# Performance work log

Measured on AMD Instinct MI355X. Metric: run time of the kernel, lower is better.

Reference implementation:

```python
import jax, jax.numpy as jnp
import numpy as np
from jax import lax

DIM, HEADS, WS = 256, 8, 8
B, H, W = 2, 192, 192


def conv1x1(x, w, b):
    # x: (b,c,h,w), w: (o,c)
    return jnp.einsum('bchw,oc->bohw', x, w) + b[None, :, None, None]


def dwconv3x3(x, w, b):
    # w: (C,1,3,3), zeros padding (padding_mode='zeros')
    y = lax.conv_general_dilated(x, w, (1, 1), ((1, 1), (1, 1)),
                                 dimension_numbers=('NCHW', 'OIHW', 'NCHW'),
                                 feature_group_count=x.shape[1])
    return y + b[None, :, None, None]


def window_split(qkv):
    # (b, 3*heads*c, H, W) -> (3, b*h1*w1, heads, c, ws*ws)
    b, C3, h, w = qkv.shape
    c = C3 // (3 * HEADS)
    h1, w1 = h // WS, w // WS
    t = qkv.reshape(b, 3, HEADS, c, h1, WS, w1, WS)
    t = t.transpose(1, 0, 4, 6, 2, 3, 5, 7)  # (3,b,h1,w1,heads,c,ws,ws)
    return t.reshape(3, b * h1 * w1, HEADS, c, WS * WS)


def window_merge(o, b, h, w):
    # (b*h1*w1, heads, c, ws*ws) -> (b, heads*c, h, w)
    h1, w1 = h // WS, w // WS
    c = o.shape[2]
    t = o.reshape(b, h1, w1, HEADS, c, WS, WS)
    t = t.transpose(0, 3, 4, 1, 5, 2, 6)  # (b,heads,c,h1,ws,w1,ws)
    return t.reshape(b, HEADS * c, h, w)


def l2norm(x):
    n = jnp.linalg.norm(x, axis=-1, keepdims=True)
    return x / jnp.maximum(n, 1e-12)


def setup_inputs() -> dict:
    key = jax.random.key(0)
    ks = jax.random.split(key, 16)
    s = 0.02
    return {
        'x': jax.random.normal(ks[0], (B, DIM, H, W), jnp.float32),
        'x2': jax.random.normal(ks[1], (B, DIM, H, W), jnp.float32),
        'w_qkv': jax.random.normal(ks[2], (3 * DIM, DIM), jnp.float32) * s,
        'b_qkv': jnp.zeros((3 * DIM,), jnp.float32),
        'w_dw': jax.random.normal(ks[3], (3 * DIM, 1, 3, 3), jnp.float32) * s,
        'b_dw': jnp.zeros((3 * DIM,), jnp.float32),
        'w_qkv2': jax.random.normal(ks[4], (3 * DIM, DIM), jnp.float32) * s,
        'b_qkv2': jnp.zeros((3 * DIM,), jnp.float32),
        'w_dw2': jax.random.normal(ks[5], (3 * DIM, 1, 3, 3), jnp.float32) * s,
        'b_dw2': jnp.zeros((3 * DIM,), jnp.float32),
        'temp': jnp.ones((HEADS, 1, 1), jnp.float32) / np.sqrt(DIM).astype(np.float32),
        'w_proj': jax.random.normal(ks[6], (DIM, DIM), jnp.float32) * s,
        'b_proj': jnp.zeros((DIM,), jnp.float32),
    }


def reference(x, x2, w_qkv, b_qkv, w_dw, b_dw, w_qkv2, b_qkv2, w_dw2, b_dw2,
              temp, w_proj, b_proj):
    b, _, h, w = x.shape
    qkv = dwconv3x3(conv1x1(x, w_qkv, b_qkv), w_dw, b_dw)
    qkv2 = dwconv3x3(conv1x1(x2, w_qkv2, b_qkv2), w_dw2, b_dw2)
    # H,W divisible by window_size -> check_image_size is a no-op
    q, k, v = window_split(qkv)       # each (Bw, heads, c, N)
    q2, k2, v2 = window_split(qkv2)
    q, k = l2norm(q), l2norm(k)
    q2, k2 = l2norm(q2), l2norm(k2)
    # channel attention (cs='channel'): scores are (c x c) per window/head
    cross = jnp.einsum('whcn,whdn->whcd', q, k2) * temp  # q @ k2^T
    cross = jax.nn.softmax(cross, axis=-1)
    cross_out = jnp.einsum('whcd,whdn->whcn', cross, v2)
    out = window_merge(cross_out, b, h, w)
    return conv1x1(out, w_proj, b_proj)
```

## Files before the change

### kernel.cpp

```cpp
#include <hip/hip_runtime.h>
#include <stdint.h>

typedef unsigned short u16;
typedef __attribute__((ext_vector_type(4))) unsigned short u16x4;
typedef __attribute__((ext_vector_type(8))) short bf16x8;
typedef __attribute__((ext_vector_type(4))) float f32x4;

#define PTOT 36864
#define WIMG 192

__device__ __forceinline__ float bf2f(u16 h) {
    union { uint32_t u; float f; } v; v.u = ((uint32_t)h) << 16; return v.f;
}
__device__ __forceinline__ u16 f2bf(float f) {
    union { float f; uint32_t u; } v; v.f = f;
    uint32_t u = v.u;
    return (u16)((u + 0x7FFFu + ((u >> 16) & 1u)) >> 16);
}

#define ASYNC_COPY16(gp, lp)                                                     \
    __builtin_amdgcn_global_load_lds(                                            \
        (const __attribute__((address_space(1))) void*)(gp),                     \
        (__attribute__((address_space(3))) void*)(lp), 16, 0, 0)

__global__ __launch_bounds__(256) void k_transpose(const float* __restrict__ x,
                                                   u16* __restrict__ xt) {
    __shared__ u16 tile[64][66];
    const int tx = threadIdx.x, ty = threadIdx.y;
    const int p0 = blockIdx.x * 64, c0 = blockIdx.y * 64, b = blockIdx.z;
    const float* src = x + (size_t)b * 256 * PTOT;
    u16* dst = xt + (size_t)b * PTOT * 256;
#pragma unroll
    for (int k = 0; k < 16; ++k) {
        const int c = c0 + ty + k * 4;
        tile[ty + k * 4][tx] = f2bf(src[(size_t)c * PTOT + p0 + tx]);
    }
    __syncthreads();
#pragma unroll
    for (int k = 0; k < 16; ++k) {
        const int p = p0 + ty + k * 4;
        dst[(size_t)p * 256 + c0 + tx] = tile[tx][ty + k * 4];
    }
}

__global__ void k_f2bfAll(const float* __restrict__ w_qkv,
                          const float* __restrict__ w_qkv2,
                          const float* __restrict__ w_proj,
                          u16* __restrict__ dst) {
    const int i = blockIdx.x * 256 + threadIdx.x;
    float v;
    if (i < 65536) v = w_qkv[i];
    else if (i < 196608) v = w_qkv2[i];
    else v = w_proj[i - 196608];
    dst[i] = f2bf(v);
}

template <bool OUT_F32>
__global__ __launch_bounds__(256) void k_gemm(const u16* __restrict__ A,
                                              const u16* __restrict__ Bt,
                                              void* __restrict__ Cout,
                                              const float* __restrict__ bias,
                                              int M) {
    __shared__ u16 As[128 * 32];
    __shared__ u16 Bs[128 * 32];
    const int tid = threadIdx.x;
    const int lane = tid & 63;
    const int wave = tid >> 6;
    const int wr = wave >> 1, wc = wave & 1;
    const int nb = blockIdx.x, mb = blockIdx.y, b = blockIdx.z;

    const u16* Ab = A + (size_t)(mb * 128) * 256;
    const u16* Bb = Bt + ((size_t)b * PTOT + (size_t)nb * 128) * 256;

    const int lrow = lane >> 2;
    const int lcol = (lane & 3) * 8;
    const int lr = lane & 15;
    const int lk = lane >> 4;

    f32x4 acc[4][4];
#pragma unroll
    for (int m = 0; m < 4; ++m)
#pragma unroll
        for (int n = 0; n < 4; ++n) acc[m][n] = (f32x4)0.f;

    for (int k0 = 0; k0 < 256; k0 += 32) {
        __syncthreads();
        const int i0 = wave * 2;
#pragma unroll
        for (int ii = 0; ii < 2; ++ii) {
            const int i = i0 + ii;
            ASYNC_COPY16(Ab + (size_t)(i * 16 + lrow) * 256 + k0 + lcol,
                         As + i * 16 * 32);
            ASYNC_COPY16(Bb + (size_t)(i * 16 + lrow) * 256 + k0 + lcol,
                         Bs + i * 16 * 32);
        }
        __syncthreads();
        const bf16x8* Asv = (const bf16x8*)As;
        const bf16x8* Bsv = (const bf16x8*)Bs;
        bf16x8 afr[4], bfr[4];
#pragma unroll
        for (int m = 0; m < 4; ++m)
            afr[m] = Asv[(wr * 64 + m * 16 + lr) * 4 + lk];
#pragma unroll
        for (int n = 0; n < 4; ++n)
            bfr[n] = Bsv[(wc * 64 + n * 16 + lr) * 4 + lk];
#pragma unroll
        for (int m = 0; m < 4; ++m)
#pragma unroll
            for (int n = 0; n < 4; ++n)
                acc[m][n] = __builtin_amdgcn_mfma_f32_16x16x32_bf16(
                    afr[m], bfr[n], acc[m][n], 0, 0, 0);
    }

    const int cr = (lane >> 4) * 4;
    const int cc = lane & 15;
#pragma unroll
    for (int m = 0; m < 4; ++m) {
#pragma unroll
        for (int j = 0; j < 4; ++j) {
            const int row = mb * 128 + wr * 64 + m * 16 + cr + j;
            const float bv = bias[row];
            const size_t rbase =
                ((size_t)b * M + row) * PTOT + (size_t)nb * 128 + wc * 64 + cc;
#pragma unroll
            for (int n = 0; n < 4; ++n) {
                const float v = acc[m][n][j] + bv;
                if (OUT_F32)
                    ((float*)Cout)[rbase + n * 16] = v;
                else
                    ((u16*)Cout)[rbase + n * 16] = f2bf(v);
            }
        }
    }
}

__global__ __launch_bounds__(256) void k_dwconv(const u16* __restrict__ in,
                                                u16* __restrict__ out,
                                                const float* __restrict__ w,
                                                const float* __restrict__ bias,
                                                int C) {
    const int vec = blockIdx.x * 256 + threadIdx.x;
    const int ch = blockIdx.y, b = blockIdx.z;
    const int yg = vec / 24, xv = vec - yg * 24;
    const int y0 = yg * 2;
    const size_t base = ((size_t)(b * C + ch)) * PTOT;
    const float* wc9 = w + ch * 9;

    float p[4][10];
#pragma unroll
    for (int r = 0; r < 4; ++r) {
        const int yy = y0 - 1 + r;
        if ((unsigned)yy >= (unsigned)WIMG) {
#pragma unroll
            for (int i = 0; i < 10; ++i) p[r][i] = 0.f;
        } else {
            const u16* row = in + base + (size_t)yy * WIMG + xv * 8;
            const bf16x8 cv = *(const bf16x8*)row;
            p[r][0] = (xv > 0) ? bf2f(row[-1]) : 0.f;
            p[r][9] = (xv < 23) ? bf2f(row[8]) : 0.f;
#pragma unroll
            for (int i = 0; i < 8; ++i) p[r][i + 1] = bf2f((u16)cv[i]);
        }
    }

    const float bv = bias[ch];
#pragma unroll
    for (int r = 0; r < 2; ++r) {
        float acc[8];
#pragma unroll
        for (int i = 0; i < 8; ++i) acc[i] = bv;
#pragma unroll
        for (int dy = 0; dy < 3; ++dy) {
            const float wa = wc9[dy * 3], wbv = wc9[dy * 3 + 1], wcv = wc9[dy * 3 + 2];
            const float* pr = p[r + dy];
#pragma unroll
            for (int i = 0; i < 8; ++i)
                acc[i] += wa * pr[i] + wbv * pr[i + 1] + wcv * pr[i + 2];
        }
        bf16x8 ov;
#pragma unroll
        for (int i = 0; i < 8; ++i) ov[i] = (short)f2bf(acc[i]);
        *(bf16x8*)(out + base + (size_t)(y0 + r) * WIMG + xv * 8) = ov;
    }
}

__global__ __launch_bounds__(256) void k_attn(const u16* __restrict__ q,
                                              const u16* __restrict__ kv,
                                              const float* __restrict__ temp,
                                              u16* __restrict__ outt) {
    __shared__ __align__(16) u16 lds[19232];
    u16* VT = lds;
    float* SS = (float*)(lds + 10272);
    u16* P = lds + 10272;
    float* IQ = (float*)(lds + 18720);
    float* IK = (float*)(lds + 18976);

    const int tid = threadIdx.x;
    const int lane = tid & 63;
    const int wv = tid >> 6;
    const int h = blockIdx.y, b = blockIdx.z;
    const int wy = blockIdx.x / 6, wxg = blockIdx.x % 6;
    const int px0 = wxg * 32;
    const int lr = lane & 15, lk = lane >> 4;

    const size_t qbase = ((size_t)b * 256 + h * 32) * PTOT;
    const size_t kbase = ((size_t)b * 512 + h * 32) * PTOT;
    const size_t vbase = kbase + (size_t)256 * PTOT;

    bf16x8 aq[2][2], bk[2][2];
#pragma unroll
    for (int kb = 0; kb < 2; ++kb) {
        const int rloc = kb * 4 + lk;
        const size_t gp = (size_t)(wy * 8 + rloc) * WIMG + px0 + wv * 8;
#pragma unroll
        for (int half = 0; half < 2; ++half) {
            const int ch = half * 16 + lr;
            aq[kb][half] = *(const bf16x8*)(q + qbase + (size_t)ch * PTOT + gp);
            bk[kb][half] = *(const bf16x8*)(kv + kbase + (size_t)ch * PTOT + gp);
        }
    }

    {
        float sq0 = 0.f, sq1 = 0.f, sk0 = 0.f, sk1 = 0.f;
#pragma unroll
        for (int kb = 0; kb < 2; ++kb)
#pragma unroll
            for (int j = 0; j < 8; ++j) {
                float a0 = bf2f((u16)aq[kb][0][j]), a1 = bf2f((u16)aq[kb][1][j]);
                float k0 = bf2f((u16)bk[kb][0][j]), k1 = bf2f((u16)bk[kb][1][j]);
                sq0 += a0 * a0; sq1 += a1 * a1;
                sk0 += k0 * k0; sk1 += k1 * k1;
            }
        sq0 += __shfl_xor(sq0, 16); sq0 += __shfl_xor(sq0, 32);
        sq1 += __shfl_xor(sq1, 16); sq1 += __shfl_xor(sq1, 32);
        sk0 += __shfl_xor(sk0, 16); sk0 += __shfl_xor(sk0, 32);
        sk1 += __shfl_xor(sk1, 16); sk1 += __shfl_xor(sk1, 32);
        if (lk == 0) {
            IQ[wv * 32 + lr]      = 1.f / fmaxf(sqrtf(sq0), 1e-12f);
            IQ[wv * 32 + 16 + lr] = 1.f / fmaxf(sqrtf(sq1), 1e-12f);
            IK[wv * 32 + lr]      = 1.f / fmaxf(sqrtf(sk0), 1e-12f);
            IK[wv * 32 + 16 + lr] = 1.f / fmaxf(sqrtf(sk1), 1e-12f);
        }
    }

#pragma unroll
    for (int it = 0; it < 4; ++it) {
        const int L = it * 256 + tid;
        const int c = L >> 5, rem = L & 31, rr = rem >> 2, w = rem & 3;
        const size_t gp = (size_t)(wy * 8 + rr) * WIMG + px0 + w * 8;
        bf16x8 vv = *(const bf16x8*)(kv + vbase + (size_t)c * PTOT + gp);
        const int blk = (c >> 3) ^ (rr & 3);
        u16* vt = VT + w * 2568 + (rr * 8) * 40 + blk * 8 + (c & 7);
#pragma unroll
        for (int j = 0; j < 8; ++j) vt[j * 40] = (u16)vv[j];
    }
    __syncthreads();

    {
        f32x4 s00 = (f32x4)0.f, s01 = (f32x4)0.f, s10 = (f32x4)0.f, s11 = (f32x4)0.f;
#pragma unroll
        for (int kb = 0; kb < 2; ++kb) {
            s00 = __builtin_amdgcn_mfma_f32_16x16x32_bf16(aq[kb][0], bk[kb][0], s00, 0, 0, 0);
            s01 = __builtin_amdgcn_mfma_f32_16x16x32_bf16(aq[kb][0], bk[kb][1], s01, 0, 0, 0);
            s10 = __builtin_amdgcn_mfma_f32_16x16x32_bf16(aq[kb][1], bk[kb][0], s10, 0, 0, 0);
            s11 = __builtin_amdgcn_mfma_f32_16x16x32_bf16(aq[kb][1], bk[kb][1], s11, 0, 0, 0);
        }
        float* srow = SS + wv * 1056;
        const int cr = lk * 4, cc = lr;
#pragma unroll
        for (int j = 0; j < 4; ++j) {
            srow[(cr + j) * 33 + cc] = s00[j];
            srow[(cr + j) * 33 + 16 + cc] = s01[j];
            srow[(16 + cr + j) * 33 + cc] = s10[j];
            srow[(16 + cr + j) * 33 + 16 + cc] = s11[j];
        }
    }
    __syncthreads();

    float sv[32];
    float pinv = 0.f;
    const int sw = tid >> 5, sc = tid & 31;
    if (tid < 128) {
        const float* srow = SS + sw * 1056 + sc * 33;
        const float* ik = IK + sw * 32;
        const float iq = IQ[sw * 32 + sc] * temp[h];
        float mx = -1e30f;
#pragma unroll
        for (int d = 0; d < 32; ++d) {
            sv[d] = srow[d] * ik[d] * iq;
            mx = fmaxf(mx, sv[d]);
        }
        float sum = 0.f;
#pragma unroll
        for (int d = 0; d < 32; ++d) {
            sv[d] = __expf(sv[d] - mx);
            sum += sv[d];
        }
        pinv = 1.f / sum;
    }
    __syncthreads();
    if (tid < 128) {
        u16* prow = P + sw * 1280 + sc * 40;
#pragma unroll
        for (int ch = 0; ch < 4; ++ch) {
            bf16x8 pv;
#pragma unroll
            for (int i = 0; i < 8; ++i) pv[i] = (short)f2bf(sv[ch * 8 + i] * pinv);
            *(bf16x8*)(prow + ch * 8) = pv;
        }
    }
    __syncthreads();

    {
        bf16x8 pa0 = *(const bf16x8*)(P + wv * 1280 + lr * 40 + lk * 8);
        bf16x8 pa1 = *(const bf16x8*)(P + wv * 1280 + (16 + lr) * 40 + lk * 8);
        f32x4 o0[4], o1[4];
#pragma unroll
        for (int ni = 0; ni < 4; ++ni) { o0[ni] = (f32x4)0.f; o1[ni] = (f32x4)0.f; }
#pragma unroll
        for (int ni = 0; ni < 4; ++ni) {
            const int n = ni * 16 + lr;
            const int blkr = lk ^ ((ni * 2 + (lr >> 3)) & 3);
            bf16x8 vb = *(const bf16x8*)(VT + wv * 2568 + n * 40 + blkr * 8);
            o0[ni] = __builtin_amdgcn_mfma_f32_16x16x32_bf16(pa0, vb, o0[ni], 0, 0, 0);
            o1[ni] = __builtin_amdgcn_mfma_f32_16x16x32_bf16(pa1, vb, o1[ni], 0, 0, 0);
        }
#pragma unroll
        for (int ni = 0; ni < 4; ++ni) {
            const int n = ni * 16 + lr;
            const size_t gp = (size_t)(wy * 8 + (n >> 3)) * WIMG + px0 + wv * 8 + (n & 7);
            u16* op = outt + ((size_t)b * PTOT + gp) * 256 + h * 32;
            u16x4 pk0, pk1;
#pragma unroll
            for (int j = 0; j < 4; ++j) { pk0[j] = f2bf(o0[ni][j]); pk1[j] = f2bf(o1[ni][j]); }
            *(u16x4*)(op + lk * 4) = pk0;
            *(u16x4*)(op + 16 + lk * 4) = pk1;
        }
    }
}

extern "C" void kernel_launch(void* const* d_in, const int* in_sizes, int n_in,
                              void* d_out, int out_size, void* d_ws, size_t ws_size,
                              hipStream_t stream) {
    (void)in_sizes; (void)n_in; (void)out_size; (void)ws_size;
    const float* x      = (const float*)d_in[0];
    const float* x2     = (const float*)d_in[1];
    const float* w_qkv  = (const float*)d_in[2];
    const float* b_qkv  = (const float*)d_in[3];
    const float* w_dw   = (const float*)d_in[4];
    const float* b_dw   = (const float*)d_in[5];
    const float* w_qkv2 = (const float*)d_in[6];
    const float* b_qkv2 = (const float*)d_in[7];
    const float* w_dw2  = (const float*)d_in[8];
    const float* b_dw2  = (const float*)d_in[9];
    const float* temp   = (const float*)d_in[10];
    const float* w_proj = (const float*)d_in[11];
    const float* b_proj = (const float*)d_in[12];
    float* out = (float*)d_out;

    char* ws = (char*)d_ws;
    const size_t SZ_T  = (size_t)2 * PTOT * 256 * 2;
    const size_t SZ_KV = (size_t)2 * PTOT * 512 * 2;
    u16* xt     = (u16*)(ws);
    u16* x2t    = (u16*)(ws + SZ_T);
    u16* qpre   = (u16*)(ws + 2 * SZ_T);
    u16* kvpre  = (u16*)(ws + 3 * SZ_T);
    u16* kvconv = (u16*)(ws + 3 * SZ_T + SZ_KV);
    u16* wq     = (u16*)(ws + 3 * SZ_T + 2 * SZ_KV);
    u16* wkv    = wq + 256 * 256;
    u16* wproj  = wkv + 512 * 256;
    u16* qconv  = xt;
    u16* attnt  = x2t;

    const dim3 tb(64, 4);
    k_transpose<<<dim3(PTOT / 64, 4, 2), tb, 0, stream>>>(x, xt);
    k_transpose<<<dim3(PTOT / 64, 4, 2), tb, 0, stream>>>(x2, x2t);
    k_f2bfAll<<<262144 / 256, 256, 0, stream>>>(w_qkv, w_qkv2, w_proj, wq);

    k_gemm<false><<<dim3(PTOT / 128, 2, 2), 256, 0, stream>>>(wq, xt, qpre, b_qkv, 256);
    k_gemm<false><<<dim3(PTOT / 128, 4, 2), 256, 0, stream>>>(wkv, x2t, kvpre, b_qkv2 + 256, 512);

    k_dwconv<<<dim3(2304 / 256, 256, 2), 256, 0, stream>>>(qpre, qconv, w_dw, b_dw, 256);
    k_dwconv<<<dim3(2304 / 256, 512, 2), 256, 0, stream>>>(kvpre, kvconv, w_dw2 + 256 * 9, b_dw2 + 256, 512);

    k_attn<<<dim3(144, 8, 2), 256, 0, stream>>>(qconv, kvconv, temp, attnt);

    k_gemm<true><<<dim3(PTOT / 128, 2, 2), 256, 0, stream>>>(wproj, attnt, out, b_proj, 256);
}
```

Baseline: 241.1 us.

## Emit dwconv output in per-window MFMA fragment layout and simplify attention

The two depthwise conv launches are merged into one kernel that writes q, k and v directly in a per-window, fragment-ordered layout (v pre-transposed), so the attention kernel can load MFMA operands straight from global memory. This removes the LDS transpose of V and a block-wide barrier in attention. Each wave now handles its own window and runs softmax independently. The two input transposes are also merged into one launch. The trade-off is more load redundancy in the dwconv (each thread reads 3 rows per output row) and scattered 2-byte stores for the v path.

```diff
diff --git a/kernel.cpp b/kernel.cpp
--- a/kernel.cpp
+++ b/kernel.cpp
@@ -24,12 +24,15 @@
         (__attribute__((address_space(3))) void*)(lp), 16, 0, 0)
 
 __global__ __launch_bounds__(256) void k_transpose(const float* __restrict__ x,
-                                                   u16* __restrict__ xt) {
+                                                   const float* __restrict__ x2,
+                                                   u16* __restrict__ xt,
+                                                   u16* __restrict__ x2t) {
     __shared__ u16 tile[64][66];
     const int tx = threadIdx.x, ty = threadIdx.y;
-    const int p0 = blockIdx.x * 64, c0 = blockIdx.y * 64, b = blockIdx.z;
-    const float* src = x + (size_t)b * 256 * PTOT;
-    u16* dst = xt + (size_t)b * PTOT * 256;
+    const int p0 = blockIdx.x * 64, c0 = blockIdx.y * 64;
+    const int z = blockIdx.z, b = z & 1;
+    const float* src = (z < 2 ? x : x2) + (size_t)b * 256 * PTOT;
+    u16* dst = (z < 2 ? xt : x2t) + (size_t)b * PTOT * 256;
 #pragma unroll
     for (int k = 0; k < 16; ++k) {
         const int c = c0 + ty + k * 4;
@@ -134,91 +137,114 @@
     }
 }
 
-__global__ __launch_bounds__(256) void k_dwconv(const u16* __restrict__ in,
-                                                u16* __restrict__ out,
-                                                const float* __restrict__ w,
-                                                const float* __restrict__ bias,
-                                                int C) {
-    const int vec = blockIdx.x * 256 + threadIdx.x;
-    const int ch = blockIdx.y, b = blockIdx.z;
-    const int yg = vec / 24, xv = vec - yg * 24;
-    const int y0 = yg * 2;
-    const size_t base = ((size_t)(b * C + ch)) * PTOT;
-    const float* wc9 = w + ch * 9;
-
-    float p[4][10];
-#pragma unroll
-    for (int r = 0; r < 4; ++r) {
-        const int yy = y0 - 1 + r;
-        if ((unsigned)yy >= (unsigned)WIMG) {
-#pragma unroll
-            for (int i = 0; i < 10; ++i) p[r][i] = 0.f;
+__global__ __launch_bounds__(256) void k_dwfrag(const u16* __restrict__ qpre,
+                                                const u16* __restrict__ kvpre,
+                                                const float* __restrict__ w_dw,
+                                                const float* __restrict__ b_dw,
+                                                const float* __restrict__ w_dw2,
+                                                const float* __restrict__ b_dw2,
+                                                u16* __restrict__ qw,
+                                                u16* __restrict__ kw,
+                                                u16* __restrict__ vw) {
+    const int tid = threadIdx.x;
+    const int c = tid >> 3, pxg = tid & 7;
+    const int bx3 = blockIdx.x % 3, wy = blockIdx.x / 3;
+    const int slab = blockIdx.y, b = blockIdx.z;
+    const int path = slab >> 3, hh = slab & 7;
+    const int ch = hh * 32 + c;
+
+    const u16* src;
+    const float* wp;
+    float bias;
+    u16* dst;
+    if (path == 0) {
+        src = qpre + ((size_t)b * 256 + ch) * PTOT;
+        wp = w_dw + ch * 9; bias = b_dw[ch]; dst = qw;
+    } else if (path == 1) {
+        src = kvpre + ((size_t)b * 512 + ch) * PTOT;
+        wp = w_dw2 + (256 + ch) * 9; bias = b_dw2[256 + ch]; dst = kw;
+    } else {
+        src = kvpre + ((size_t)b * 512 + 256 + ch) * PTOT;
+        wp = w_dw2 + (512 + ch) * 9; bias = b_dw2[512 + ch]; dst = vw;
+    }
+    float w9[9];
+#pragma unroll
+    for (int i = 0; i < 9; ++i) w9[i] = wp[i];
+
+    const int x0 = bx3 * 64 + pxg * 8;
+    const size_t winbase =
+        (((size_t)b * 8 + hh) * 576 + (size_t)wy * 24 + bx3 * 8 + pxg) * 2048;
+
+#pragma unroll
+    for (int y = 0; y < 8; ++y) {
+        const int gy = wy * 8 + y;
+        float acc[8];
+#pragma unroll
+        for (int i = 0; i < 8; ++i) acc[i] = bias;
+#pragma unroll
+        for (int dy = 0; dy < 3; ++dy) {
+            const int yy = gy + dy - 1;
+            if ((unsigned)yy >= (unsigned)WIMG) continue;
+            const u16* row = src + (size_t)yy * WIMG + x0;
+            const bf16x8 cv = *(const bf16x8*)row;
+            float p[10];
+            p[0] = (x0 > 0) ? bf2f(row[-1]) : 0.f;
+            p[9] = (x0 < 184) ? bf2f(row[8]) : 0.f;
+#pragma unroll
+            for (int i = 0; i < 8; ++i) p[i + 1] = bf2f((u16)cv[i]);
+            const float wa = w9[dy * 3], wbv = w9[dy * 3 + 1], wcv = w9[dy * 3 + 2];
+#pragma unroll
+            for (int i = 0; i < 8; ++i)
+                acc[i] += wa * p[i] + wbv * p[i + 1] + wcv * p[i + 2];
+        }
+        if (path < 2) {
+            bf16x8 ov;
+#pragma unroll
+            for (int i = 0; i < 8; ++i) ov[i] = (short)f2bf(acc[i]);
+            *(bf16x8*)(dst + winbase + y * 256 + c * 8) = ov;
         } else {
-            const u16* row = in + base + (size_t)yy * WIMG + xv * 8;
-            const bf16x8 cv = *(const bf16x8*)row;
-            p[r][0] = (xv > 0) ? bf2f(row[-1]) : 0.f;
-            p[r][9] = (xv < 23) ? bf2f(row[8]) : 0.f;
-#pragma unroll
-            for (int i = 0; i < 8; ++i) p[r][i + 1] = bf2f((u16)cv[i]);
-        }
-    }
-
-    const float bv = bias[ch];
-#pragma unroll
-    for (int r = 0; r < 2; ++r) {
-        float acc[8];
-#pragma unroll
-        for (int i = 0; i < 8; ++i) acc[i] = bv;
-#pragma unroll
-        for (int dy = 0; dy < 3; ++dy) {
-            const float wa = wc9[dy * 3], wbv = wc9[dy * 3 + 1], wcv = wc9[dy * 3 + 2];
-            const float* pr = p[r + dy];
-#pragma unroll
-            for (int i = 0; i < 8; ++i)
-                acc[i] += wa * pr[i] + wbv * pr[i + 1] + wcv * pr[i + 2];
-        }
-        bf16x8 ov;
-#pragma unroll
-        for (int i = 0; i < 8; ++i) ov[i] = (short)f2bf(acc[i]);
-        *(bf16x8*)(out + base + (size_t)(y0 + r) * WIMG + xv * 8) = ov;
-    }
-}
-
-__global__ __launch_bounds__(256) void k_attn(const u16* __restrict__ q,
-                                              const u16* __restrict__ kv,
+#pragma unroll
+            for (int j = 0; j < 8; ++j)
+                dst[winbase + (y * 8 + j) * 32 + c] = f2bf(acc[j]);
+        }
+    }
+}
+
+__global__ __launch_bounds__(256) void k_attn(const u16* __restrict__ qw,
+                                              const u16* __restrict__ kw,
+                                              const u16* __restrict__ vw,
                                               const float* __restrict__ temp,
                                               u16* __restrict__ outt) {
-    __shared__ __align__(16) u16 lds[19232];
-    u16* VT = lds;
-    float* SS = (float*)(lds + 10272);
-    u16* P = lds + 10272;
-    float* IQ = (float*)(lds + 18720);
-    float* IK = (float*)(lds + 18976);
+    __shared__ __align__(16) char lds[28160];
+    float* SS = (float*)lds;
+    u16* P = (u16*)(lds + 16896);
+    float* IQ = (float*)(lds + 27136);
+    float* IK = (float*)(lds + 27648);
 
     const int tid = threadIdx.x;
     const int lane = tid & 63;
     const int wv = tid >> 6;
     const int h = blockIdx.y, b = blockIdx.z;
-    const int wy = blockIdx.x / 6, wxg = blockIdx.x % 6;
-    const int px0 = wxg * 32;
+    const int win_lin = blockIdx.x * 4 + wv;
+    const int wy = win_lin / 24, wxc = win_lin % 24;
     const int lr = lane & 15, lk = lane >> 4;
 
-    const size_t qbase = ((size_t)b * 256 + h * 32) * PTOT;
-    const size_t kbase = ((size_t)b * 512 + h * 32) * PTOT;
-    const size_t vbase = kbase + (size_t)256 * PTOT;
-
-    bf16x8 aq[2][2], bk[2][2];
+    const size_t fb = (((size_t)b * 8 + h) * 576 + win_lin) * 2048;
+
+    bf16x8 aq[2][2], bk[2][2], vb[4];
 #pragma unroll
     for (int kb = 0; kb < 2; ++kb) {
-        const int rloc = kb * 4 + lk;
-        const size_t gp = (size_t)(wy * 8 + rloc) * WIMG + px0 + wv * 8;
+        const int roff = (kb * 4 + lk) * 256;
 #pragma unroll
         for (int half = 0; half < 2; ++half) {
-            const int ch = half * 16 + lr;
-            aq[kb][half] = *(const bf16x8*)(q + qbase + (size_t)ch * PTOT + gp);
-            bk[kb][half] = *(const bf16x8*)(kv + kbase + (size_t)ch * PTOT + gp);
-        }
-    }
+            const int coff = (half * 16 + lr) * 8;
+            aq[kb][half] = *(const bf16x8*)(qw + fb + roff + coff);
+            bk[kb][half] = *(const bf16x8*)(kw + fb + roff + coff);
+        }
+    }
+#pragma unroll
+    for (int ni = 0; ni < 4; ++ni)
+        vb[ni] = *(const bf16x8*)(vw + fb + (ni * 16 + lr) * 32 + lk * 8);
 
     {
         float sq0 = 0.f, sq1 = 0.f, sk0 = 0.f, sk1 = 0.f;
@@ -243,19 +269,6 @@
         }
     }
 
-#pragma unroll
-    for (int it = 0; it < 4; ++it) {
-        const int L = it * 256 + tid;
-        const int c = L >> 5, rem = L & 31, rr = rem >> 2, w = rem & 3;
-        const size_t gp = (size_t)(wy * 8 + rr) * WIMG + px0 + w * 8;
-        bf16x8 vv = *(const bf16x8*)(kv + vbase + (size_t)c * PTOT + gp);
-        const int blk = (c >> 3) ^ (rr & 3);
-        u16* vt = VT + w * 2568 + (rr * 8) * 40 + blk * 8 + (c & 7);
-#pragma unroll
-        for (int j = 0; j < 8; ++j) vt[j * 40] = (u16)vv[j];
-    }
-    __syncthreads();
-
     {
         f32x4 s00 = (f32x4)0.f, s01 = (f32x4)0.f, s10 = (f32x4)0.f, s11 = (f32x4)0.f;
 #pragma unroll
@@ -277,13 +290,11 @@
     }
     __syncthreads();
 
-    float sv[32];
-    float pinv = 0.f;
-    const int sw = tid >> 5, sc = tid & 31;
-    if (tid < 128) {
-        const float* srow = SS + sw * 1056 + sc * 33;
-        const float* ik = IK + sw * 32;
-        const float iq = IQ[sw * 32 + sc] * temp[h];
+    if (lane < 32) {
+        const float* srow = SS + wv * 1056 + lane * 33;
+        const float* ik = IK + wv * 32;
+        const float iq = IQ[wv * 32 + lane] * temp[h];
+        float sv[32];
         float mx = -1e30f;
 #pragma unroll
         for (int d = 0; d < 32; ++d) {
@@ -296,11 +307,8 @@
             sv[d] = __expf(sv[d] - mx);
             sum += sv[d];
         }
-        pinv = 1.f / sum;
-    }
-    __syncthreads();
-    if (tid < 128) {
-        u16* prow = P + sw * 1280 + sc * 40;
+        const float pinv = 1.f / sum;
+        u16* prow = P + wv * 1280 + lane * 40;
 #pragma unroll
         for (int ch = 0; ch < 4; ++ch) {
             bf16x8 pv;
@@ -319,16 +327,13 @@
         for (int ni = 0; ni < 4; ++ni) { o0[ni] = (f32x4)0.f; o1[ni] = (f32x4)0.f; }
 #pragma unroll
         for (int ni = 0; ni < 4; ++ni) {
-            const int n = ni * 16 + lr;
-            const int blkr = lk ^ ((ni * 2 + (lr >> 3)) & 3);
-            bf16x8 vb = *(const bf16x8*)(VT + wv * 2568 + n * 40 + blkr * 8);
-            o0[ni] = __builtin_amdgcn_mfma_f32_16x16x32_bf16(pa0, vb, o0[ni], 0, 0, 0);
-            o1[ni] = __builtin_amdgcn_mfma_f32_16x16x32_bf16(pa1, vb, o1[ni], 0, 0, 0);
+            o0[ni] = __builtin_amdgcn_mfma_f32_16x16x32_bf16(pa0, vb[ni], o0[ni], 0, 0, 0);
+            o1[ni] = __builtin_amdgcn_mfma_f32_16x16x32_bf16(pa1, vb[ni], o1[ni], 0, 0, 0);
         }
 #pragma unroll
         for (int ni = 0; ni < 4; ++ni) {
             const int n = ni * 16 + lr;
-            const size_t gp = (size_t)(wy * 8 + (n >> 3)) * WIMG + px0 + wv * 8 + (n & 7);
+            const size_t gp = (size_t)(wy * 8 + (n >> 3)) * WIMG + wxc * 8 + (n & 7);
             u16* op = outt + ((size_t)b * PTOT + gp) * 256 + h * 32;
             u16x4 pk0, pk1;
 #pragma unroll
@@ -365,25 +370,25 @@
     u16* x2t    = (u16*)(ws + SZ_T);
     u16* qpre   = (u16*)(ws + 2 * SZ_T);
     u16* kvpre  = (u16*)(ws + 3 * SZ_T);
-    u16* kvconv = (u16*)(ws + 3 * SZ_T + SZ_KV);
-    u16* wq     = (u16*)(ws + 3 * SZ_T + 2 * SZ_KV);
+    u16* vw     = (u16*)(ws + 3 * SZ_T + SZ_KV);
+    u16* wq     = (u16*)(ws + 4 * SZ_T + SZ_KV);
     u16* wkv    = wq + 256 * 256;
     u16* wproj  = wkv + 512 * 256;
-    u16* qconv  = xt;
-    u16* attnt  = x2t;
+    u16* qw     = xt;
+    u16* kw     = x2t;
+    u16* attnt  = qpre;
 
     const dim3 tb(64, 4);
-    k_transpose<<<dim3(PTOT / 64, 4, 2), tb, 0, stream>>>(x, xt);
-    k_transpose<<<dim3(PTOT / 64, 4, 2), tb, 0, stream>>>(x2, x2t);
+    k_transpose<<<dim3(PTOT / 64, 4, 4), tb, 0, stream>>>(x, x2, xt, x2t);
     k_f2bfAll<<<262144 / 256, 256, 0, stream>>>(w_qkv, w_qkv2, w_proj, wq);
 
     k_gemm<false><<<dim3(PTOT / 128, 2, 2), 256, 0, stream>>>(wq, xt, qpre, b_qkv, 256);
     k_gemm<false><<<dim3(PTOT / 128, 4, 2), 256, 0, stream>>>(wkv, x2t, kvpre, b_qkv2 + 256, 512);
 
-    k_dwconv<<<dim3(2304 / 256, 256, 2), 256, 0, stream>>>(qpre, qconv, w_dw, b_dw, 256);
-    k_dwconv<<<dim3(2304 / 256, 512, 2), 256, 0, stream>>>(kvpre, kvconv, w_dw2 + 256 * 9, b_dw2 + 256, 512);
-
-    k_attn<<<dim3(144, 8, 2), 256, 0, stream>>>(qconv, kvconv, temp, attnt);
+    k_dwfrag<<<dim3(72, 24, 2), 256, 0, stream>>>(qpre, kvpre, w_dw, b_dw,
+                                                  w_dw2, b_dw2, qw, kw, vw);
+
+    k_attn<<<dim3(144, 8, 2), 256, 0, stream>>>(qw, kw, vw, temp, attnt);
 
     k_gemm<true><<<dim3(PTOT / 128, 2, 2), 256, 0, stream>>>(wproj, attnt, out, b_proj, 256);
 }
```

After: 278.2 us. 1.15x slower.
